# Kernel optimization log

Measured on AMD Instinct MI355X. Metric: run time of the kernel, lower is better.

## Reference

```python
import jax, jax.numpy as jnp
import numpy as np

EPS = 1e-8

def setup_inputs() -> dict:
    key = jax.random.key(0)
    k1, k2 = jax.random.split(key)
    B, N, M, D = 8, 4096, 4096, 3
    x1 = jax.random.normal(k1, (B, N, D), dtype=jnp.float32)
    y1 = jax.random.normal(k2, (B, M, D), dtype=jnp.float32)
    return {"x1": x1, "y1": y1}

def reference(x1, y1):
    # Faithful to: dist = sqrt(1e-8 + sum((x1[:,None,:,:] - y1[:,:,None,:])**2, -1))
    # computed via the Gram-matrix expansion to avoid the (B,M,N,D) intermediate.
    x_sq = jnp.sum(x1 * x1, axis=-1)                 # (B, N)
    y_sq = jnp.sum(y1 * y1, axis=-1)                 # (B, M)
    xy = jnp.einsum('bmd,bnd->bmn', y1, x1)          # (B, M, N)
    d2 = jnp.maximum(y_sq[:, :, None] + x_sq[:, None, :] - 2.0 * xy, 0.0)
    dist = jnp.sqrt(EPS + d2)                        # (B, M, N)
    min1 = jnp.min(dist, axis=1)                     # (B, N): nearest y for each x
    min2 = jnp.min(dist, axis=2)                     # (B, M): nearest x for each y
    return jnp.mean(min1) + jnp.mean(min2)
```

## Files before the change

kernel.cpp:

```cpp
#include <hip/hip_runtime.h>

constexpr int B = 8;
constexpr int N = 4096;
constexpr int PTS = B * N;
constexpr int TOT = 2 * PTS;

#define TPB 256
#define R 16
#define RP (R / 2)
#define CHUNK 128
#define KC (N / CHUNK)

typedef float float2v __attribute__((ext_vector_type(2)));

__global__ __launch_bounds__(TPB) void chamfer_min5(
        const float* __restrict__ x1, const float* __restrict__ y1,
        float* __restrict__ partials,
        float* __restrict__ out) {
    __shared__ float4 qs[CHUNK];

    if (blockIdx.x == 0 && blockIdx.y == 0 && blockIdx.z == 0 && threadIdx.x == 0)
        out[0] = 0.0f;

    const int chunk = blockIdx.x;
    const int dir   = blockIdx.y;
    const int b     = blockIdx.z;

    const float* own = dir ? y1 : x1;
    const float* oth = dir ? x1 : y1;

    if (threadIdx.x < CHUNK) {
        const float* op = oth + ((size_t)b * N + chunk * CHUNK + threadIdx.x) * 3;
        float qx = op[0], qy = op[1], qz = op[2];
        qs[threadIdx.x] = make_float4(qx, qy, qz, fmaf(qx, qx, fmaf(qy, qy, qz * qz)));
    }

    float2v mx2[RP], my2[RP], mz2[RP], acc2[RP];
    float xx[R];
    #pragma unroll
    for (int p = 0; p < RP; p++) {
        #pragma unroll
        for (int e = 0; e < 2; e++) {
            const int r = 2 * p + e;
            const float* pp = own + ((size_t)b * N + threadIdx.x + r * TPB) * 3;
            float px = pp[0], py = pp[1], pz = pp[2];
            mx2[p][e] = -2.0f * px;
            my2[p][e] = -2.0f * py;
            mz2[p][e] = -2.0f * pz;
            xx[r] = fmaf(px, px, fmaf(py, py, pz * pz));
        }
        acc2[p] = float2v{3.4e38f, 3.4e38f};
    }

    __syncthreads();

    #pragma unroll 2
    for (int j = 0; j < CHUNK; j += 2) {
        union { float4 f4; float2v f2[2]; } qa0, qa1;
        qa0.f4 = qs[j];
        qa1.f4 = qs[j + 1];
        float2v xy0 = qa0.f2[0], zw0 = qa0.f2[1];
        float2v xy1 = qa1.f2[0], zw1 = qa1.f2[1];
        #pragma unroll
        for (int p = 0; p < RP; p++) {
            float2v g0, g1;
            asm("v_pk_fma_f32 %0, %1, %2, %1 op_sel:[0,0,1] op_sel_hi:[0,1,1]"
                : "=v"(g0) : "v"(zw0), "v"(mz2[p]));
            asm("v_pk_fma_f32 %0, %1, %2, %1 op_sel:[0,0,1] op_sel_hi:[0,1,1]"
                : "=v"(g1) : "v"(zw1), "v"(mz2[p]));
            asm("v_pk_fma_f32 %0, %1, %2, %3 op_sel:[1,0,0] op_sel_hi:[1,1,1]"
                : "=v"(g0) : "v"(xy0), "v"(my2[p]), "v"(g0));
            asm("v_pk_fma_f32 %0, %1, %2, %3 op_sel:[1,0,0] op_sel_hi:[1,1,1]"
                : "=v"(g1) : "v"(xy1), "v"(my2[p]), "v"(g1));
            asm("v_pk_fma_f32 %0, %1, %2, %3 op_sel:[0,0,0] op_sel_hi:[0,1,1]"
                : "=v"(g0) : "v"(xy0), "v"(mx2[p]), "v"(g0));
            asm("v_pk_fma_f32 %0, %1, %2, %3 op_sel:[0,0,0] op_sel_hi:[0,1,1]"
                : "=v"(g1) : "v"(xy1), "v"(mx2[p]), "v"(g1));
            acc2[p].x = fminf(fminf(acc2[p].x, g0.x), g1.x);
            acc2[p].y = fminf(fminf(acc2[p].y, g0.y), g1.y);
        }
    }

    float* dst = partials + (size_t)chunk * TOT + (size_t)dir * PTS + (size_t)b * N;
    #pragma unroll
    for (int p = 0; p < RP; p++) {
        dst[threadIdx.x + (2 * p) * TPB]     = fmaxf(acc2[p].x + xx[2 * p], 0.0f);
        dst[threadIdx.x + (2 * p + 1) * TPB] = fmaxf(acc2[p].y + xx[2 * p + 1], 0.0f);
    }
}

__global__ __launch_bounds__(256) void chamfer_finish(
        const float* __restrict__ partials, float* __restrict__ out, float scale) {
    int p = blockIdx.x * 256 + threadIdx.x;
    float m = partials[p];
    #pragma unroll
    for (int c = 1; c < KC; c++) m = fminf(m, partials[(size_t)c * TOT + p]);
    float s = sqrtf(1e-8f + m) * scale;

    #pragma unroll
    for (int off = 32; off > 0; off >>= 1) s += __shfl_down(s, off, 64);

    __shared__ float partial[4];
    const int wid = threadIdx.x >> 6, lane = threadIdx.x & 63;
    if (lane == 0) partial[wid] = s;
    __syncthreads();
    if (threadIdx.x == 0) {
        atomicAdd(out, partial[0] + partial[1] + partial[2] + partial[3]);
    }
}

extern "C" void kernel_launch(void* const* d_in, const int* in_sizes, int n_in,
                              void* d_out, int out_size, void* d_ws, size_t ws_size,
                              hipStream_t stream) {
    const float* x1 = (const float*)d_in[0];
    const float* y1 = (const float*)d_in[1];
    float* out = (float*)d_out;

    float* partials = (float*)d_ws;

    dim3 grid(KC, 2, B);
    chamfer_min5<<<grid, TPB, 0, stream>>>(x1, y1, partials, out);

    chamfer_finish<<<TOT / 256, 256, 0, stream>>>(partials, out, 1.0f / (B * N));
}
```

Baseline: 82.06 us.

## Fuse min and mean into one kernel with in-block split-query reduction

Each block now owns 128 points spread as 8 slots × 16 points. Its 256 threads split the full 4096-point opposite set into 32 subranges, staged through padded shared memory in two 2048-point halves. Partial minima are reduced with cross-lane shuffles and shared memory, and each block adds its scaled sqrt sum to the output with an atomic. This removes the large partials buffer round trip and the second finish kernel. In exchange it adds intra-block reductions, a memset launch, and fewer blocks (512) with a large LDS footprint.

```diff
diff --git a/kernel.cpp b/kernel.cpp
--- a/kernel.cpp
+++ b/kernel.cpp
@@ -1,125 +1,146 @@
 #include <hip/hip_runtime.h>
+
 
 constexpr int B = 8;
 constexpr int N = 4096;
-constexpr int PTS = B * N;
-constexpr int TOT = 2 * PTS;
 
 #define TPB 256
-#define R 16
-#define RP (R / 2)
-#define CHUNK 128
-#define KC (N / CHUNK)
+#define OWN 128
+#define RP 8
+#define NSP 32
+#define CH 2048
+#define SPLEN (CH / NSP)
 
 typedef float float2v __attribute__((ext_vector_type(2)));
 
-__global__ __launch_bounds__(TPB) void chamfer_min5(
+__global__ __launch_bounds__(TPB, 2) void chamfer_fused(
         const float* __restrict__ x1, const float* __restrict__ y1,
-        float* __restrict__ partials,
-        float* __restrict__ out) {
-    __shared__ float4 qs[CHUNK];
+        float* __restrict__ out, float scale) {
+    __shared__ float4 qs[CH + CH / 64];
+    __shared__ float red[4 * OWN];
+    __shared__ float wsum[4];
 
-    if (blockIdx.x == 0 && blockIdx.y == 0 && blockIdx.z == 0 && threadIdx.x == 0)
-        out[0] = 0.0f;
+    const int tid  = threadIdx.x;
+    const int tile = blockIdx.x;
+    const int dir  = blockIdx.y;
+    const int b    = blockIdx.z;
 
-    const int chunk = blockIdx.x;
-    const int dir   = blockIdx.y;
-    const int b     = blockIdx.z;
+    const float* own = (dir ? y1 : x1) + (size_t)b * N * 3;
+    const float* oth = (dir ? x1 : y1) + (size_t)b * N * 3;
+    const float2* o2 = (const float2*)oth;
 
-    const float* own = dir ? y1 : x1;
-    const float* oth = dir ? x1 : y1;
+    const int slot = tid & 7;
+    const int sp   = tid >> 3;
 
-    if (threadIdx.x < CHUNK) {
-        const float* op = oth + ((size_t)b * N + chunk * CHUNK + threadIdx.x) * 3;
-        float qx = op[0], qy = op[1], qz = op[2];
-        qs[threadIdx.x] = make_float4(qx, qy, qz, fmaf(qx, qx, fmaf(qy, qy, qz * qz)));
+    float2v mx2[RP], my2[RP], mz2[RP], xx2[RP], acc2[RP];
+    {
+        const float2* p2 = (const float2*)(own + (size_t)(tile * OWN + slot * 16) * 3);
+        #pragma unroll
+        for (int p = 0; p < RP; p++) {
+            float2 a = p2[3 * p], d = p2[3 * p + 1], e = p2[3 * p + 2];
+            mx2[p] = float2v{-2.0f * a.x, -2.0f * d.y};
+            my2[p] = float2v{-2.0f * a.y, -2.0f * e.x};
+            mz2[p] = float2v{-2.0f * d.x, -2.0f * e.y};
+            xx2[p] = float2v{fmaf(a.x, a.x, fmaf(a.y, a.y, d.x * d.x)),
+                             fmaf(d.y, d.y, fmaf(e.x, e.x, e.y * e.y))};
+            acc2[p] = float2v{3.4e38f, 3.4e38f};
+        }
     }
 
-    float2v mx2[RP], my2[RP], mz2[RP], acc2[RP];
-    float xx[R];
+    for (int c = 0; c < 2; c++) {
+        if (c) __syncthreads();
+        #pragma unroll
+        for (int k = 0; k < 4; k++) {
+            int u = tid + k * TPB;
+            float2 a = o2[c * 3072 + 3 * u];
+            float2 d = o2[c * 3072 + 3 * u + 1];
+            float2 e = o2[c * 3072 + 3 * u + 2];
+            int i0 = 2 * u, i1 = 2 * u + 1;
+            qs[i0 + (i0 >> 6)] = make_float4(a.x, a.y, d.x,
+                    fmaf(a.x, a.x, fmaf(a.y, a.y, d.x * d.x)));
+            qs[i1 + (i1 >> 6)] = make_float4(d.y, e.x, e.y,
+                    fmaf(d.y, d.y, fmaf(e.x, e.x, e.y * e.y)));
+        }
+        __syncthreads();
+
+        const float4* q = qs + sp * (SPLEN + 1);
+        #pragma unroll 4
+        for (int j = 0; j < SPLEN; j += 2) {
+            union { float4 f4; float2v f2[2]; } qa0, qa1;
+            qa0.f4 = q[j];
+            qa1.f4 = q[j + 1];
+            float2v xy0 = qa0.f2[0], zw0 = qa0.f2[1];
+            float2v xy1 = qa1.f2[0], zw1 = qa1.f2[1];
+            #pragma unroll
+            for (int p = 0; p < RP; p++) {
+                float2v g0, g1;
+                asm("v_pk_fma_f32 %0, %1, %2, %1 op_sel:[0,0,1] op_sel_hi:[0,1,1]"
+                    : "=v"(g0) : "v"(zw0), "v"(mz2[p]));
+                asm("v_pk_fma_f32 %0, %1, %2, %1 op_sel:[0,0,1] op_sel_hi:[0,1,1]"
+                    : "=v"(g1) : "v"(zw1), "v"(mz2[p]));
+                asm("v_pk_fma_f32 %0, %1, %2, %3 op_sel:[1,0,0] op_sel_hi:[1,1,1]"
+                    : "=v"(g0) : "v"(xy0), "v"(my2[p]), "v"(g0));
+                asm("v_pk_fma_f32 %0, %1, %2, %3 op_sel:[1,0,0] op_sel_hi:[1,1,1]"
+                    : "=v"(g1) : "v"(xy1), "v"(my2[p]), "v"(g1));
+                asm("v_pk_fma_f32 %0, %1, %2, %3 op_sel:[0,0,0] op_sel_hi:[0,1,1]"
+                    : "=v"(g0) : "v"(xy0), "v"(mx2[p]), "v"(g0));
+                asm("v_pk_fma_f32 %0, %1, %2, %3 op_sel:[0,0,0] op_sel_hi:[0,1,1]"
+                    : "=v"(g1) : "v"(xy1), "v"(mx2[p]), "v"(g1));
+                acc2[p].x = fminf(fminf(acc2[p].x, g0.x), g1.x);
+                acc2[p].y = fminf(fminf(acc2[p].y, g0.y), g1.y);
+            }
+        }
+    }
+
+    #pragma unroll
+    for (int p = 0; p < RP; p++) acc2[p] += xx2[p];
+
+    const int lane = tid & 63;
+    const int wid  = tid >> 6;
     #pragma unroll
     for (int p = 0; p < RP; p++) {
         #pragma unroll
         for (int e = 0; e < 2; e++) {
-            const int r = 2 * p + e;
-            const float* pp = own + ((size_t)b * N + threadIdx.x + r * TPB) * 3;
-            float px = pp[0], py = pp[1], pz = pp[2];
-            mx2[p][e] = -2.0f * px;
-            my2[p][e] = -2.0f * py;
-            mz2[p][e] = -2.0f * pz;
-            xx[r] = fmaf(px, px, fmaf(py, py, pz * pz));
+            float v = acc2[p][e];
+            v = fminf(v, __shfl_xor(v, 8, 64));
+            v = fminf(v, __shfl_xor(v, 16, 64));
+            v = fminf(v, __shfl_xor(v, 32, 64));
+            acc2[p][e] = v;
         }
-        acc2[p] = float2v{3.4e38f, 3.4e38f};
     }
-
+    if (lane < 8) {
+        #pragma unroll
+        for (int p = 0; p < RP; p++) {
+            red[wid * OWN + lane * 16 + 2 * p]     = acc2[p].x;
+            red[wid * OWN + lane * 16 + 2 * p + 1] = acc2[p].y;
+        }
+    }
     __syncthreads();
 
-    #pragma unroll 2
-    for (int j = 0; j < CHUNK; j += 2) {
-        union { float4 f4; float2v f2[2]; } qa0, qa1;
-        qa0.f4 = qs[j];
-        qa1.f4 = qs[j + 1];
-        float2v xy0 = qa0.f2[0], zw0 = qa0.f2[1];
-        float2v xy1 = qa1.f2[0], zw1 = qa1.f2[1];
-        #pragma unroll
-        for (int p = 0; p < RP; p++) {
-            float2v g0, g1;
-            asm("v_pk_fma_f32 %0, %1, %2, %1 op_sel:[0,0,1] op_sel_hi:[0,1,1]"
-                : "=v"(g0) : "v"(zw0), "v"(mz2[p]));
-            asm("v_pk_fma_f32 %0, %1, %2, %1 op_sel:[0,0,1] op_sel_hi:[0,1,1]"
-                : "=v"(g1) : "v"(zw1), "v"(mz2[p]));
-            asm("v_pk_fma_f32 %0, %1, %2, %3 op_sel:[1,0,0] op_sel_hi:[1,1,1]"
-                : "=v"(g0) : "v"(xy0), "v"(my2[p]), "v"(g0));
-            asm("v_pk_fma_f32 %0, %1, %2, %3 op_sel:[1,0,0] op_sel_hi:[1,1,1]"
-                : "=v"(g1) : "v"(xy1), "v"(my2[p]), "v"(g1));
-            asm("v_pk_fma_f32 %0, %1, %2, %3 op_sel:[0,0,0] op_sel_hi:[0,1,1]"
-                : "=v"(g0) : "v"(xy0), "v"(mx2[p]), "v"(g0));
-            asm("v_pk_fma_f32 %0, %1, %2, %3 op_sel:[0,0,0] op_sel_hi:[0,1,1]"
-                : "=v"(g1) : "v"(xy1), "v"(mx2[p]), "v"(g1));
-            acc2[p].x = fminf(fminf(acc2[p].x, g0.x), g1.x);
-            acc2[p].y = fminf(fminf(acc2[p].y, g0.y), g1.y);
-        }
+    float s = 0.0f;
+    if (tid < OWN) {
+        float m = fminf(fminf(red[tid], red[OWN + tid]),
+                        fminf(red[2 * OWN + tid], red[3 * OWN + tid]));
+        s = sqrtf(1e-8f + fmaxf(m, 0.0f));
     }
-
-    float* dst = partials + (size_t)chunk * TOT + (size_t)dir * PTS + (size_t)b * N;
-    #pragma unroll
-    for (int p = 0; p < RP; p++) {
-        dst[threadIdx.x + (2 * p) * TPB]     = fmaxf(acc2[p].x + xx[2 * p], 0.0f);
-        dst[threadIdx.x + (2 * p + 1) * TPB] = fmaxf(acc2[p].y + xx[2 * p + 1], 0.0f);
-    }
-}
-
-__global__ __launch_bounds__(256) void chamfer_finish(
-        const float* __restrict__ partials, float* __restrict__ out, float scale) {
-    int p = blockIdx.x * 256 + threadIdx.x;
-    float m = partials[p];
-    #pragma unroll
-    for (int c = 1; c < KC; c++) m = fminf(m, partials[(size_t)c * TOT + p]);
-    float s = sqrtf(1e-8f + m) * scale;
-
     #pragma unroll
     for (int off = 32; off > 0; off >>= 1) s += __shfl_down(s, off, 64);
-
-    __shared__ float partial[4];
-    const int wid = threadIdx.x >> 6, lane = threadIdx.x & 63;
-    if (lane == 0) partial[wid] = s;
+    if (lane == 0) wsum[wid] = s;
     __syncthreads();
-    if (threadIdx.x == 0) {
-        atomicAdd(out, partial[0] + partial[1] + partial[2] + partial[3]);
-    }
+    if (tid == 0)
+        atomicAdd(out, (wsum[0] + wsum[1] + wsum[2] + wsum[3]) * scale);
 }
 
 extern "C" void kernel_launch(void* const* d_in, const int* in_sizes, int n_in,
                               void* d_out, int out_size, void* d_ws, size_t ws_size,
                               hipStream_t stream) {
+    (void)in_sizes; (void)n_in; (void)d_ws; (void)ws_size; (void)out_size;
     const float* x1 = (const float*)d_in[0];
     const float* y1 = (const float*)d_in[1];
-    float* out = (float*)d_out;
 
-    float* partials = (float*)d_ws;
+    hipMemsetAsync(d_out, 0, sizeof(float), stream);
 
-    dim3 grid(KC, 2, B);
-    chamfer_min5<<<grid, TPB, 0, stream>>>(x1, y1, partials, out);
-
-    chamfer_finish<<<TOT / 256, 256, 0, stream>>>(partials, out, 1.0f / (B * N));
+    dim3 grid(N / OWN, 2, B);
+    chamfer_fused<<<grid, TPB, 0, stream>>>(x1, y1, (float*)d_out,
+                                            1.0f / (B * N));
 }
```

Measured after the change: 81.05 us. No clear change (-1.2%).
